# Kernel tuning notes

Hardware: AMD Instinct MI355X
Metric: run time of the kernel (lower is better)

Reference implementation:

```python
import jax, jax.numpy as jnp
import numpy as np

N, E, T = 10000, 50000, 80000   # nodes, edges, triplets
D, H, C, CF = 16, 128, 64, 64   # n_orb, hidden_dim, conv_dim, coeffs_dim


def l2norm(v):
    # matches torch F.normalize(dim=-1): x / max(||x||_2, 1e-12)
    return v / jnp.maximum(jnp.linalg.norm(v, axis=-1, keepdims=True), 1e-12)


def setup_inputs() -> dict:
    key = jax.random.key(0)
    ks = jax.random.split(key, 16)

    def w(k, i, o):
        return jax.random.normal(k, (i, o), jnp.float32) / np.sqrt(i).astype(np.float32)

    return {
        "x": jax.random.normal(ks[0], (N, H), jnp.float32),
        "cji": jax.random.normal(ks[1], (E, D, CF), jnp.float32),
        "robs": jax.random.normal(ks[2], (E, D), jnp.float32),
        "shbs": jax.random.normal(ks[3], (T, D), jnp.float32),
        "idx_i": jax.random.randint(ks[4], (E,), 0, N),
        "idx_j": jax.random.randint(ks[5], (E,), 0, N),
        "tri_idx_k": jax.random.randint(ks[6], (T,), 0, N),
        "edge_idx_kj": jax.random.randint(ks[7], (T,), 0, E),
        "edge_idx_ji": jax.random.randint(ks[8], (T,), 0, E),
        "W_nb": w(ks[9], H, 2 * C), "b_nb": jnp.zeros((2 * C,), jnp.float32),
        "W_c1": w(ks[10], CF, C),
        "W_c2": w(ks[11], C, 2 * C),
        "W_t3": w(ks[12], C, C), "b_t3": jnp.zeros((C,), jnp.float32),
        "W_n1": w(ks[13], 2 * C, C), "b_n1": jnp.zeros((C,), jnp.float32),
        "W_n2": w(ks[14], C, C), "b_n2": jnp.zeros((C,), jnp.float32),
        "W_na": w(ks[15], C, H),
    }


def reference(x, cji, robs, shbs, idx_i, idx_j, tri_idx_k, edge_idx_kj,
              edge_idx_ji, W_nb, b_nb, W_c1, W_c2, W_t3, b_t3, W_n1, b_n1,
              W_n2, b_n2, W_na):
    silu = jax.nn.silu
    # node_before_lin + chunk
    h = x @ W_nb + b_nb                       # [N, 2C]
    xq, xk = jnp.split(h, 2, axis=-1)         # each [N, C]
    # coeffs_before_lin: act -> Dense -> act -> Dense (no biases)
    c = silu(silu(cji) @ W_c1) @ W_c2         # [E, D, 2C]
    cji2, ckj = jnp.split(c, 2, axis=-1)      # each [E, D, C]
    # triplet gathers
    ckj_g = l2norm(ckj[edge_idx_kj])          # [T, D, C]
    tbo = l2norm(jnp.einsum('td,tdh->th', shbs * robs[edge_idx_kj], ckj_g))  # [T, C]
    tbw = tbo * jax.nn.sigmoid(xk[tri_idx_k])  # [T, C]
    # scatter triplets -> edges (dim_size = robs.size(0) = E)
    agg = jax.ops.segment_sum(tbw, edge_idx_ji, num_segments=E)  # [E, C]
    tbw2 = silu(agg) @ W_t3 + b_t3            # three_lin, [E, C]
    cji3 = l2norm(cji2 * (1.0 + tbw2[:, None, :]))  # cji + cji*w, normalized
    lcao = l2norm(jnp.einsum('ed,edh->eh', robs, cji3))  # [E, C]
    # node message: node_lin on concatenated endpoint features
    m = jnp.concatenate([xq[idx_i], xq[idx_j]], axis=-1)  # [E, 2C]
    m = silu(silu(m) @ W_n1 + b_n1) @ W_n2 + b_n2          # [E, C]
    out = x + jax.ops.segment_sum(lcao * m, idx_i, num_segments=N) @ W_na
    return out
```

## Files before the change

### kernel.cpp

```cpp
#include <hip/hip_runtime.h>
#include <hip/hip_bf16.h>

#define NN 10000
#define EE 50000
#define TT 80000
#define DD 16
#define HH 128
#define CC 64

typedef __hip_bfloat16 bf16;
typedef __attribute__((ext_vector_type(8))) short bf16x8;
typedef __attribute__((ext_vector_type(4))) float f32x4;

__device__ __forceinline__ float silu_f(float x) {
  return x * __builtin_amdgcn_rcpf(1.f + __expf(-x));
}
__device__ __forceinline__ float sigm_f(float x) {
  return __builtin_amdgcn_rcpf(1.f + __expf(-x));
}

__device__ __forceinline__ short f2bs(float x) {
  __hip_bfloat16 h = __float2bfloat16(x);
  short s;
  __builtin_memcpy(&s, &h, 2);
  return s;
}

__device__ __forceinline__ float rnorm_f(float ss) {
  return __builtin_amdgcn_rcpf(fmaxf(__builtin_amdgcn_sqrtf(ss), 1e-12f));
}

__device__ __forceinline__ void bf2x(unsigned u, float& lo, float& hi) {
  lo = __uint_as_float(u << 16);
  hi = __uint_as_float(u & 0xffff0000u);
}

#define ZERO_U4 960000
__global__ __launch_bounds__(256) void k_zero(uint4* __restrict__ p) {
  const int stride = gridDim.x * 256;
  for (int i = blockIdx.x * 256 + threadIdx.x; i < ZERO_U4; i += stride)
    p[i] = (uint4){0u, 0u, 0u, 0u};
}

__global__ __launch_bounds__(128) void k_node(
    const float* __restrict__ x, const float* __restrict__ W_nb,
    const float* __restrict__ b_nb, float* __restrict__ sxq,
    float* __restrict__ sigxk) {
  __shared__ __align__(16) float xs[8][HH];
  const int t = threadIdx.x;
  const int base = blockIdx.x * 8;
#pragma unroll
  for (int i = 0; i < 8; ++i) xs[i][t] = x[(size_t)(base + i) * HH + t];
  __syncthreads();
  float acc[8];
  const float bb = b_nb[t];
#pragma unroll
  for (int i = 0; i < 8; ++i) acc[i] = bb;
  for (int k = 0; k < HH; k += 4) {
    const float w0 = W_nb[(k + 0) * HH + t];
    const float w1 = W_nb[(k + 1) * HH + t];
    const float w2 = W_nb[(k + 2) * HH + t];
    const float w3 = W_nb[(k + 3) * HH + t];
#pragma unroll
    for (int i = 0; i < 8; ++i) {
      const float4 xv = *(const float4*)(&xs[i][k]);
      acc[i] = fmaf(xv.x, w0, acc[i]);
      acc[i] = fmaf(xv.y, w1, acc[i]);
      acc[i] = fmaf(xv.z, w2, acc[i]);
      acc[i] = fmaf(xv.w, w3, acc[i]);
    }
  }
  if (t < CC) {
#pragma unroll
    for (int i = 0; i < 8; ++i)
      sxq[(size_t)(base + i) * CC + t] = silu_f(acc[i]);
  } else {
#pragma unroll
    for (int i = 0; i < 8; ++i)
      sigxk[(size_t)(base + i) * CC + (t - CC)] = sigm_f(acc[i]);
  }
}

#define K2_BLOCKS 2048
#define K2_TILES 50000
__global__ __launch_bounds__(256, 2) void k_coeffs(
    const float* __restrict__ cji, const float* __restrict__ W_c1,
    const float* __restrict__ W_c2, bf16* __restrict__ cji2,
    bf16* __restrict__ ckjn) {
  __shared__ __align__(16) short xbuf[4][16 * 72];
  const int tid = threadIdx.x;
  const int w = tid >> 6, l = tid & 63;
  const int lr = l & 15, lg = l >> 4;
  short* mybuf = xbuf[w];

  bf16x8 b1[2][4];
  bf16x8 b2[2][8];
#pragma unroll
  for (int kt = 0; kt < 2; ++kt) {
#pragma unroll
    for (int nt = 0; nt < 4; ++nt) {
      bf16x8 t;
#pragma unroll
      for (int b = 0; b < 8; ++b)
        t[b] = f2bs(W_c1[(kt * 32 + lg * 8 + b) * 64 + nt * 16 + lr]);
      b1[kt][nt] = t;
    }
#pragma unroll
    for (int nt = 0; nt < 8; ++nt) {
      bf16x8 t;
#pragma unroll
      for (int b = 0; b < 8; ++b)
        t[b] = f2bs(W_c2[(kt * 32 + lg * 8 + b) * 128 + nt * 16 + lr]);
      b2[kt][nt] = t;
    }
  }

  const int nwave = K2_BLOCKS * 4;
  int tile = blockIdx.x * 4 + w;
  if (tile >= K2_TILES) return;

  float4 r0, r1, r2, r3;
  {
    const float* Ab = cji + (size_t)tile * 1024 + lr * 64 + lg * 8;
    r0 = *(const float4*)(Ab);
    r1 = *(const float4*)(Ab + 4);
    r2 = *(const float4*)(Ab + 32);
    r3 = *(const float4*)(Ab + 36);
  }

  for (; tile < K2_TILES; tile += nwave) {
    bf16x8 a0, a1;
    a0[0] = f2bs(silu_f(r0.x)); a0[1] = f2bs(silu_f(r0.y));
    a0[2] = f2bs(silu_f(r0.z)); a0[3] = f2bs(silu_f(r0.w));
    a0[4] = f2bs(silu_f(r1.x)); a0[5] = f2bs(silu_f(r1.y));
    a0[6] = f2bs(silu_f(r1.z)); a0[7] = f2bs(silu_f(r1.w));
    a1[0] = f2bs(silu_f(r2.x)); a1[1] = f2bs(silu_f(r2.y));
    a1[2] = f2bs(silu_f(r2.z)); a1[3] = f2bs(silu_f(r2.w));
    a1[4] = f2bs(silu_f(r3.x)); a1[5] = f2bs(silu_f(r3.y));
    a1[6] = f2bs(silu_f(r3.z)); a1[7] = f2bs(silu_f(r3.w));

    const int next = tile + nwave;
    if (next < K2_TILES) {
      const float* Ab = cji + (size_t)next * 1024 + lr * 64 + lg * 8;
      r0 = *(const float4*)(Ab);
      r1 = *(const float4*)(Ab + 4);
      r2 = *(const float4*)(Ab + 32);
      r3 = *(const float4*)(Ab + 36);
    }

    f32x4 acc1[4];
#pragma unroll
    for (int nt = 0; nt < 4; ++nt) acc1[nt] = (f32x4){0.f, 0.f, 0.f, 0.f};
#pragma unroll
    for (int nt = 0; nt < 4; ++nt) {
      acc1[nt] = __builtin_amdgcn_mfma_f32_16x16x32_bf16(a0, b1[0][nt], acc1[nt], 0, 0, 0);
      acc1[nt] = __builtin_amdgcn_mfma_f32_16x16x32_bf16(a1, b1[1][nt], acc1[nt], 0, 0, 0);
    }

#pragma unroll
    for (int nt = 0; nt < 4; ++nt)
#pragma unroll
      for (int j = 0; j < 4; ++j)
        mybuf[(lg * 4 + j) * 72 + nt * 16 + lr] = f2bs(silu_f(acc1[nt][j]));

    const bf16x8 a20 = *(const bf16x8*)(mybuf + lr * 72 + lg * 8);
    const bf16x8 a21 = *(const bf16x8*)(mybuf + lr * 72 + 32 + lg * 8);

    f32x4 acc2[8];
#pragma unroll
    for (int nt = 0; nt < 8; ++nt) acc2[nt] = (f32x4){0.f, 0.f, 0.f, 0.f};
#pragma unroll
    for (int nt = 0; nt < 8; ++nt) {
      acc2[nt] = __builtin_amdgcn_mfma_f32_16x16x32_bf16(a20, b2[0][nt], acc2[nt], 0, 0, 0);
      acc2[nt] = __builtin_amdgcn_mfma_f32_16x16x32_bf16(a21, b2[1][nt], acc2[nt], 0, 0, 0);
    }

    float rn[4];
#pragma unroll
    for (int j = 0; j < 4; ++j) {
      float ss = acc2[4][j] * acc2[4][j];
      ss = fmaf(acc2[5][j], acc2[5][j], ss);
      ss = fmaf(acc2[6][j], acc2[6][j], ss);
      ss = fmaf(acc2[7][j], acc2[7][j], ss);
#pragma unroll
      for (int m = 1; m < 16; m <<= 1) ss += __shfl_xor(ss, m, 64);
      rn[j] = rnorm_f(ss);
    }

    union { short h[16]; uint4 u[2]; } p;
#pragma unroll
    for (int nt = 0; nt < 4; ++nt)
#pragma unroll
      for (int j = 0; j < 4; ++j) p.h[nt * 4 + j] = f2bs(acc2[nt][j]);
    {
      uint4* d0 = (uint4*)(cji2 + (size_t)tile * 1024 + l * 16);
      d0[0] = p.u[0];
      d0[1] = p.u[1];
    }
#pragma unroll
    for (int nt = 0; nt < 4; ++nt)
#pragma unroll
      for (int j = 0; j < 4; ++j) p.h[nt * 4 + j] = f2bs(acc2[4 + nt][j] * rn[j]);
    {
      uint4* d1 = (uint4*)(ckjn + (size_t)tile * 1024 + l * 16);
      d1[0] = p.u[0];
      d1[1] = p.u[1];
    }
  }
}

#define K3_WAVES 20000
__global__ __launch_bounds__(256) void k_triplet(
    const bf16* __restrict__ ckjn, const float* __restrict__ shbs,
    const float* __restrict__ robs, const float* __restrict__ sigxk,
    const int* __restrict__ tri_idx_k, const int* __restrict__ edge_idx_kj,
    const int* __restrict__ edge_idx_ji, float* __restrict__ agg) {
  const int wid = (blockIdx.x * 256 + threadIdx.x) >> 6;
  const int l = threadIdx.x & 63;
  if (wid >= K3_WAVES) return;
  const int lq = l >> 4;
  const int t0 = wid * 4;

  int kj[4], kn[4], ji[4];
#pragma unroll
  for (int i = 0; i < 4; ++i) {
    kj[i] = edge_idx_kj[t0 + i];
    kn[i] = tri_idx_k[t0 + i];
    ji[i] = edge_idx_ji[t0 + i];
  }
  float4 sh[4], rb[4];
  uint4 u0[4], u1[4];
  float sx[4];
#pragma unroll
  for (int i = 0; i < 4; ++i) {
    sh[i] = *(const float4*)(shbs + (size_t)(t0 + i) * DD + lq * 4);
    rb[i] = *(const float4*)(robs + (size_t)kj[i] * DD + lq * 4);
    const uint4* b = (const uint4*)(ckjn + (size_t)kj[i] * 1024 + l * 16);
    u0[i] = b[0];
    u1[i] = b[1];
    sx[i] = sigxk[(size_t)kn[i] * CC + l];
  }

  float acc[4][4];
#pragma unroll
  for (int i = 0; i < 4; ++i) {
    const float w0 = sh[i].x * rb[i].x, w1 = sh[i].y * rb[i].y,
                w2 = sh[i].z * rb[i].z, w3 = sh[i].w * rb[i].w;
    float x0, x1, x2, x3;
    bf2x(u0[i].x, x0, x1); bf2x(u0[i].y, x2, x3);
    acc[i][0] = fmaf(w3, x3, fmaf(w2, x2, fmaf(w1, x1, w0 * x0)));
    bf2x(u0[i].z, x0, x1); bf2x(u0[i].w, x2, x3);
    acc[i][1] = fmaf(w3, x3, fmaf(w2, x2, fmaf(w1, x1, w0 * x0)));
    bf2x(u1[i].x, x0, x1); bf2x(u1[i].y, x2, x3);
    acc[i][2] = fmaf(w3, x3, fmaf(w2, x2, fmaf(w1, x1, w0 * x0)));
    bf2x(u1[i].z, x0, x1); bf2x(u1[i].w, x2, x3);
    acc[i][3] = fmaf(w3, x3, fmaf(w2, x2, fmaf(w1, x1, w0 * x0)));
  }
#pragma unroll
  for (int m = 16; m < 64; m <<= 1)
#pragma unroll
    for (int i = 0; i < 4; ++i)
#pragma unroll
      for (int q = 0; q < 4; ++q) acc[i][q] += __shfl_xor(acc[i][q], m, 64);

  float sel[4], ss[4];
#pragma unroll
  for (int i = 0; i < 4; ++i) {
    sel[i] = (lq == 0) ? acc[i][0] : (lq == 1) ? acc[i][1]
             : (lq == 2) ? acc[i][2] : acc[i][3];
    ss[i] = sel[i] * sel[i];
  }
#pragma unroll
  for (int m = 1; m < 64; m <<= 1)
#pragma unroll
    for (int i = 0; i < 4; ++i) ss[i] += __shfl_xor(ss[i], m, 64);
#pragma unroll
  for (int i = 0; i < 4; ++i) {
    const float tbw = sel[i] * rnorm_f(ss[i]) * sx[i];
    atomicAdd(&agg[(size_t)ji[i] * CC + l], tbw);
  }
}

#define K4A_TILES 3125
#define K4A_BLOCKS 256
__global__ __launch_bounds__(256, 2) void k_edge_a(
    const float* __restrict__ agg, const float* __restrict__ sxq,
    const int* __restrict__ idx_i, const int* __restrict__ idx_j,
    const float* __restrict__ W_t3, const float* __restrict__ b_t3,
    const float* __restrict__ W_n1, const float* __restrict__ b_n1,
    const float* __restrict__ W_n2, const float* __restrict__ b_n2,
    float* __restrict__ onew_buf, float* __restrict__ m_buf) {
  __shared__ __align__(16) float fbuf[4][16 * 68];
  __shared__ __align__(16) short sbuf[4][16 * 72];
  const int tid = threadIdx.x;
  const int w = tid >> 6, l = tid & 63;
  const int lr = l & 15, lg = l >> 4;
  float* fb = fbuf[w];
  short* sb = sbuf[w];

  bf16x8 bt3[2][4], bn1[4][4], bn2[2][4];
#pragma unroll
  for (int kt = 0; kt < 2; ++kt)
#pragma unroll
    for (int nt = 0; nt < 4; ++nt) {
      bf16x8 t;
#pragma unroll
      for (int b = 0; b < 8; ++b)
        t[b] = f2bs(W_t3[(kt * 32 + lg * 8 + b) * 64 + nt * 16 + lr]);
      bt3[kt][nt] = t;
    }
#pragma unroll
  for (int kt = 0; kt < 4; ++kt)
#pragma unroll
    for (int nt = 0; nt < 4; ++nt) {
      bf16x8 t;
#pragma unroll
      for (int b = 0; b < 8; ++b)
        t[b] = f2bs(W_n1[(kt * 32 + lg * 8 + b) * 64 + nt * 16 + lr]);
      bn1[kt][nt] = t;
    }
#pragma unroll
  for (int kt = 0; kt < 2; ++kt)
#pragma unroll
    for (int nt = 0; nt < 4; ++nt) {
      bf16x8 t;
#pragma unroll
      for (int b = 0; b < 8; ++b)
        t[b] = f2bs(W_n2[(kt * 32 + lg * 8 + b) * 64 + nt * 16 + lr]);
      bn2[kt][nt] = t;
    }
  float bt3c[4], bn1c[4], bn2c[4];
#pragma unroll
  for (int nt = 0; nt < 4; ++nt) {
    bt3c[nt] = b_t3[nt * 16 + lr];
    bn1c[nt] = b_n1[nt * 16 + lr];
    bn2c[nt] = b_n2[nt * 16 + lr];
  }

  for (int tile = blockIdx.x * 4 + w; tile < K4A_TILES; tile += K4A_BLOCKS * 4) {
    const int e = tile * 16 + lr;
    const int vi = idx_i[e], vj = idx_j[e];

    bf16x8 aagg[2];
#pragma unroll
    for (int kt = 0; kt < 2; ++kt) {
      const float4 u = *(const float4*)(agg + (size_t)e * 64 + kt * 32 + lg * 8);
      const float4 v = *(const float4*)(agg + (size_t)e * 64 + kt * 32 + lg * 8 + 4);
      bf16x8 t;
      t[0] = f2bs(silu_f(u.x)); t[1] = f2bs(silu_f(u.y));
      t[2] = f2bs(silu_f(u.z)); t[3] = f2bs(silu_f(u.w));
      t[4] = f2bs(silu_f(v.x)); t[5] = f2bs(silu_f(v.y));
      t[6] = f2bs(silu_f(v.z)); t[7] = f2bs(silu_f(v.w));
      aagg[kt] = t;
    }
    f32x4 acc[4];
#pragma unroll
    for (int nt = 0; nt < 4; ++nt) acc[nt] = (f32x4){0.f, 0.f, 0.f, 0.f};
#pragma unroll
    for (int nt = 0; nt < 4; ++nt) {
      acc[nt] = __builtin_amdgcn_mfma_f32_16x16x32_bf16(aagg[0], bt3[0][nt], acc[nt], 0, 0, 0);
      acc[nt] = __builtin_amdgcn_mfma_f32_16x16x32_bf16(aagg[1], bt3[1][nt], acc[nt], 0, 0, 0);
    }
#pragma unroll
    for (int nt = 0; nt < 4; ++nt)
#pragma unroll
      for (int j = 0; j < 4; ++j)
        fb[(lg * 4 + j) * 68 + nt * 16 + lr] = 1.f + bt3c[nt] + acc[nt][j];
    {
      const int row = l >> 2, cs = (l & 3) * 16;
      float* dst = onew_buf + (size_t)(tile * 16 + row) * 64 + cs;
#pragma unroll
      for (int q = 0; q < 4; ++q)
        *(float4*)(dst + q * 4) = *(const float4*)(fb + row * 68 + cs + q * 4);
    }

    bf16x8 am[4];
#pragma unroll
    for (int kt = 0; kt < 4; ++kt) {
      const float* src = (kt < 2) ? (sxq + (size_t)vi * 64 + kt * 32)
                                  : (sxq + (size_t)vj * 64 + (kt - 2) * 32);
      const float4 u = *(const float4*)(src + lg * 8);
      const float4 v = *(const float4*)(src + lg * 8 + 4);
      bf16x8 t;
      t[0] = f2bs(u.x); t[1] = f2bs(u.y); t[2] = f2bs(u.z); t[3] = f2bs(u.w);
      t[4] = f2bs(v.x); t[5] = f2bs(v.y); t[6] = f2bs(v.z); t[7] = f2bs(v.w);
      am[kt] = t;
    }
    f32x4 acc1[4];
#pragma unroll
    for (int nt = 0; nt < 4; ++nt) acc1[nt] = (f32x4){0.f, 0.f, 0.f, 0.f};
#pragma unroll
    for (int nt = 0; nt < 4; ++nt)
#pragma unroll
      for (int kt = 0; kt < 4; ++kt)
        acc1[nt] = __builtin_amdgcn_mfma_f32_16x16x32_bf16(am[kt], bn1[kt][nt], acc1[nt], 0, 0, 0);

#pragma unroll
    for (int nt = 0; nt < 4; ++nt)
#pragma unroll
      for (int j = 0; j < 4; ++j)
        sb[(lg * 4 + j) * 72 + nt * 16 + lr] = f2bs(silu_f(acc1[nt][j] + bn1c[nt]));
    const bf16x8 a20 = *(const bf16x8*)(sb + lr * 72 + lg * 8);
    const bf16x8 a21 = *(const bf16x8*)(sb + lr * 72 + 32 + lg * 8);

    f32x4 acc2[4];
#pragma unroll
    for (int nt = 0; nt < 4; ++nt) acc2[nt] = (f32x4){0.f, 0.f, 0.f, 0.f};
#pragma unroll
    for (int nt = 0; nt < 4; ++nt) {
      acc2[nt] = __builtin_amdgcn_mfma_f32_16x16x32_bf16(a20, bn2[0][nt], acc2[nt], 0, 0, 0);
      acc2[nt] = __builtin_amdgcn_mfma_f32_16x16x32_bf16(a21, bn2[1][nt], acc2[nt], 0, 0, 0);
    }
#pragma unroll
    for (int nt = 0; nt < 4; ++nt)
#pragma unroll
      for (int j = 0; j < 4; ++j)
        fb[(lg * 4 + j) * 68 + nt * 16 + lr] = acc2[nt][j] + bn2c[nt];
    {
      const int row = l >> 2, cs = (l & 3) * 16;
      float* dst = m_buf + (size_t)(tile * 16 + row) * 64 + cs;
#pragma unroll
      for (int q = 0; q < 4; ++q)
        *(float4*)(dst + q * 4) = *(const float4*)(fb + row * 68 + cs + q * 4);
    }
  }
}

#define K4B_WAVES 25000
__global__ __launch_bounds__(256) void k_edge_b(
    const bf16* __restrict__ cji2, const float* __restrict__ robs,
    const float* __restrict__ onew_buf, const float* __restrict__ m_buf,
    const int* __restrict__ idx_i, float* __restrict__ lacc) {
  const int wid = (blockIdx.x * 256 + threadIdx.x) >> 6;
  const int l = threadIdx.x & 63;
  if (wid >= K4B_WAVES) return;
  const int lq = l >> 4, lr = l & 15;
  const int e0 = wid * 2;

  uint4 u0[2], u1[2];
  float4 rb[2];
  float ow[2][4], mm[2];
  int vi[2];
#pragma unroll
  for (int i = 0; i < 2; ++i) {
    const uint4* base = (const uint4*)(cji2 + (size_t)(e0 + i) * 1024 + l * 16);
    u0[i] = base[0];
    u1[i] = base[1];
    const float* ob = onew_buf + (size_t)(e0 + i) * 64 + lr;
    ow[i][0] = ob[0]; ow[i][1] = ob[16]; ow[i][2] = ob[32]; ow[i][3] = ob[48];
    rb[i] = *(const float4*)(robs + (size_t)(e0 + i) * DD + lq * 4);
    mm[i] = m_buf[(size_t)(e0 + i) * 64 + l];
    vi[i] = idx_i[e0 + i];
  }

  float v[2][16];
#pragma unroll
  for (int i = 0; i < 2; ++i) {
    bf2x(u0[i].x, v[i][0], v[i][1]);   bf2x(u0[i].y, v[i][2], v[i][3]);
    bf2x(u0[i].z, v[i][4], v[i][5]);   bf2x(u0[i].w, v[i][6], v[i][7]);
    bf2x(u1[i].x, v[i][8], v[i][9]);   bf2x(u1[i].y, v[i][10], v[i][11]);
    bf2x(u1[i].z, v[i][12], v[i][13]); bf2x(u1[i].w, v[i][14], v[i][15]);
#pragma unroll
    for (int j = 0; j < 4; ++j) {
      v[i][j] *= ow[i][0];
      v[i][4 + j] *= ow[i][1];
      v[i][8 + j] *= ow[i][2];
      v[i][12 + j] *= ow[i][3];
    }
  }
  float sq[2][4];
#pragma unroll
  for (int i = 0; i < 2; ++i)
#pragma unroll
    for (int j = 0; j < 4; ++j)
      sq[i][j] = fmaf(v[i][j], v[i][j],
                 fmaf(v[i][4 + j], v[i][4 + j],
                 fmaf(v[i][8 + j], v[i][8 + j], v[i][12 + j] * v[i][12 + j])));
#pragma unroll
  for (int m = 1; m < 16; m <<= 1)
#pragma unroll
    for (int i = 0; i < 2; ++i)
#pragma unroll
      for (int j = 0; j < 4; ++j) sq[i][j] += __shfl_xor(sq[i][j], m, 64);

  float lcq[2][4];
#pragma unroll
  for (int i = 0; i < 2; ++i) {
    const float t0 = rb[i].x * rnorm_f(sq[i][0]),
                t1 = rb[i].y * rnorm_f(sq[i][1]),
                t2 = rb[i].z * rnorm_f(sq[i][2]),
                t3 = rb[i].w * rnorm_f(sq[i][3]);
#pragma unroll
    for (int q = 0; q < 4; ++q)
      lcq[i][q] = fmaf(t0, v[i][q * 4 + 0],
                  fmaf(t1, v[i][q * 4 + 1],
                  fmaf(t2, v[i][q * 4 + 2], t3 * v[i][q * 4 + 3])));
  }
#pragma unroll
  for (int m = 16; m < 64; m <<= 1)
#pragma unroll
    for (int i = 0; i < 2; ++i)
#pragma unroll
      for (int q = 0; q < 4; ++q) lcq[i][q] += __shfl_xor(lcq[i][q], m, 64);

  float sel[2], ss[2];
#pragma unroll
  for (int i = 0; i < 2; ++i) {
    sel[i] = (lq == 0) ? lcq[i][0] : (lq == 1) ? lcq[i][1]
             : (lq == 2) ? lcq[i][2] : lcq[i][3];
    ss[i] = sel[i] * sel[i];
  }
#pragma unroll
  for (int m = 1; m < 64; m <<= 1)
#pragma unroll
    for (int i = 0; i < 2; ++i) ss[i] += __shfl_xor(ss[i], m, 64);
#pragma unroll
  for (int i = 0; i < 2; ++i) {
    const float lcao = sel[i] * rnorm_f(ss[i]);
    atomicAdd(&lacc[(size_t)vi[i] * CC + l], lcao * mm[i]);
  }
}

__global__ __launch_bounds__(128) void k_out(
    const float* __restrict__ x, const float* __restrict__ lacc,
    const float* __restrict__ W_na, float* __restrict__ out) {
  __shared__ __align__(16) float ls[8][CC];
  const int t = threadIdx.x;
  const int base = blockIdx.x * 8;
  for (int idx = t; idx < 8 * CC; idx += 128)
    ls[idx >> 6][idx & 63] = lacc[(size_t)(base + (idx >> 6)) * CC + (idx & 63)];
  __syncthreads();
  float acc[8];
#pragma unroll
  for (int i = 0; i < 8; ++i) acc[i] = x[(size_t)(base + i) * HH + t];
  for (int k = 0; k < CC; k += 4) {
    const float w0 = W_na[(k + 0) * HH + t];
    const float w1 = W_na[(k + 1) * HH + t];
    const float w2 = W_na[(k + 2) * HH + t];
    const float w3 = W_na[(k + 3) * HH + t];
#pragma unroll
    for (int i = 0; i < 8; ++i) {
      const float4 lv = *(const float4*)(&ls[i][k]);
      acc[i] = fmaf(lv.x, w0, acc[i]);
      acc[i] = fmaf(lv.y, w1, acc[i]);
      acc[i] = fmaf(lv.z, w2, acc[i]);
      acc[i] = fmaf(lv.w, w3, acc[i]);
    }
  }
#pragma unroll
  for (int i = 0; i < 8; ++i) out[(size_t)(base + i) * HH + t] = acc[i];
}

extern "C" void kernel_launch(void* const* d_in, const int* in_sizes, int n_in,
                              void* d_out, int out_size, void* d_ws,
                              size_t ws_size, hipStream_t stream) {
  const float* x = (const float*)d_in[0];
  const float* cji = (const float*)d_in[1];
  const float* robs = (const float*)d_in[2];
  const float* shbs = (const float*)d_in[3];
  const int* idx_i = (const int*)d_in[4];
  const int* idx_j = (const int*)d_in[5];
  const int* tri_idx_k = (const int*)d_in[6];
  const int* edge_idx_kj = (const int*)d_in[7];
  const int* edge_idx_ji = (const int*)d_in[8];
  const float* W_nb = (const float*)d_in[9];
  const float* b_nb = (const float*)d_in[10];
  const float* W_c1 = (const float*)d_in[11];
  const float* W_c2 = (const float*)d_in[12];
  const float* W_t3 = (const float*)d_in[13];
  const float* b_t3 = (const float*)d_in[14];
  const float* W_n1 = (const float*)d_in[15];
  const float* b_n1 = (const float*)d_in[16];
  const float* W_n2 = (const float*)d_in[17];
  const float* b_n2 = (const float*)d_in[18];
  const float* W_na = (const float*)d_in[19];
  float* out = (float*)d_out;

  char* ws = (char*)d_ws;
  const size_t NC4 = (size_t)NN * CC * 4;
  const size_t EDC2 = (size_t)EE * DD * CC * 2;
  const size_t EC4 = (size_t)EE * CC * 4;
  float* sxq = (float*)(ws);
  float* sigxk = (float*)(ws + NC4);
  bf16* cji2 = (bf16*)(ws + 2 * NC4);
  bf16* ckjn = (bf16*)(ws + 2 * NC4 + EDC2);
  float* agg = (float*)(ws + 2 * NC4 + 2 * EDC2);
  float* lacc = (float*)(ws + 2 * NC4 + 2 * EDC2 + EC4);
  float* onew_buf = (float*)(ws + 2 * NC4 + EDC2);
  float* m_buf = (float*)(ws + 2 * NC4 + EDC2 + EC4);

  k_zero<<<1024, 256, 0, stream>>>((uint4*)agg);

  k_node<<<NN / 8, 128, 0, stream>>>(x, W_nb, b_nb, sxq, sigxk);
  k_coeffs<<<K2_BLOCKS, 256, 0, stream>>>(cji, W_c1, W_c2, cji2, ckjn);
  k_triplet<<<(K3_WAVES + 3) / 4, 256, 0, stream>>>(ckjn, shbs, robs, sigxk,
                                                    tri_idx_k, edge_idx_kj,
                                                    edge_idx_ji, agg);
  k_edge_a<<<K4A_BLOCKS, 256, 0, stream>>>(
      agg, sxq, idx_i, idx_j, W_t3, b_t3, W_n1, b_n1, W_n2, b_n2, onew_buf,
      m_buf);
  k_edge_b<<<(K4B_WAVES + 3) / 4, 256, 0, stream>>>(cji2, robs, onew_buf,
                                                    m_buf, idx_i, lacc);
  k_out<<<NN / 8, 128, 0, stream>>>(x, lacc, W_na, out);
}
```

Baseline: 200.4 us.

## Chain coeff MLP MFMAs in registers via transposed 16x16x16 layout, drop LDS

Recasts the two-layer coefficient MLP in k_coeffs so the first GEMM computes the transposed product (W1^T times activations) with 16x16x16 bf16 MFMAs. Its accumulator layout then serves directly as the A operand of the second GEMM, which removes the per-tile LDS round trip used to re-layout the hidden activations. Input loads are reshaped to match the new K-split. The cost is twice as many, smaller MFMA instructions and changed weight-register packing, with the same overall work.

```diff
diff --git a/kernel.cpp b/kernel.cpp
--- a/kernel.cpp
+++ b/kernel.cpp
@@ -10,6 +10,7 @@
 
 typedef __hip_bfloat16 bf16;
 typedef __attribute__((ext_vector_type(8))) short bf16x8;
+typedef __attribute__((ext_vector_type(4))) short bf16x4;
 typedef __attribute__((ext_vector_type(4))) float f32x4;
 
 __device__ __forceinline__ float silu_f(float x) {
@@ -87,93 +88,87 @@
     const float* __restrict__ cji, const float* __restrict__ W_c1,
     const float* __restrict__ W_c2, bf16* __restrict__ cji2,
     bf16* __restrict__ ckjn) {
-  __shared__ __align__(16) short xbuf[4][16 * 72];
   const int tid = threadIdx.x;
   const int w = tid >> 6, l = tid & 63;
   const int lr = l & 15, lg = l >> 4;
-  short* mybuf = xbuf[w];
-
-  bf16x8 b1[2][4];
-  bf16x8 b2[2][8];
-#pragma unroll
-  for (int kt = 0; kt < 2; ++kt) {
-#pragma unroll
-    for (int nt = 0; nt < 4; ++nt) {
-      bf16x8 t;
-#pragma unroll
-      for (int b = 0; b < 8; ++b)
-        t[b] = f2bs(W_c1[(kt * 32 + lg * 8 + b) * 64 + nt * 16 + lr]);
-      b1[kt][nt] = t;
-    }
-#pragma unroll
-    for (int nt = 0; nt < 8; ++nt) {
-      bf16x8 t;
-#pragma unroll
-      for (int b = 0; b < 8; ++b)
-        t[b] = f2bs(W_c2[(kt * 32 + lg * 8 + b) * 128 + nt * 16 + lr]);
-      b2[kt][nt] = t;
-    }
-  }
+
+  bf16x4 bw1[4][4];
+  bf16x4 bw2[4][8];
+#pragma unroll
+  for (int rt = 0; rt < 4; ++rt)
+#pragma unroll
+    for (int kt = 0; kt < 4; ++kt) {
+      bf16x4 t;
+#pragma unroll
+      for (int b = 0; b < 4; ++b)
+        t[b] = f2bs(W_c1[(kt * 16 + lg * 4 + b) * 64 + rt * 16 + lr]);
+      bw1[rt][kt] = t;
+    }
+#pragma unroll
+  for (int kt = 0; kt < 4; ++kt)
+#pragma unroll
+    for (int ct = 0; ct < 8; ++ct) {
+      bf16x4 t;
+#pragma unroll
+      for (int b = 0; b < 4; ++b)
+        t[b] = f2bs(W_c2[(kt * 16 + lg * 4 + b) * 128 + ct * 16 + lr]);
+      bw2[kt][ct] = t;
+    }
 
   const int nwave = K2_BLOCKS * 4;
   int tile = blockIdx.x * 4 + w;
   if (tile >= K2_TILES) return;
 
-  float4 r0, r1, r2, r3;
-  {
-    const float* Ab = cji + (size_t)tile * 1024 + lr * 64 + lg * 8;
-    r0 = *(const float4*)(Ab);
-    r1 = *(const float4*)(Ab + 4);
-    r2 = *(const float4*)(Ab + 32);
-    r3 = *(const float4*)(Ab + 36);
-  }
+  float4 r[4];
+#pragma unroll
+  for (int kt = 0; kt < 4; ++kt)
+    r[kt] = *(const float4*)(cji + (size_t)tile * 1024 + lr * 64 + kt * 16 + lg * 4);
 
   for (; tile < K2_TILES; tile += nwave) {
-    bf16x8 a0, a1;
-    a0[0] = f2bs(silu_f(r0.x)); a0[1] = f2bs(silu_f(r0.y));
-    a0[2] = f2bs(silu_f(r0.z)); a0[3] = f2bs(silu_f(r0.w));
-    a0[4] = f2bs(silu_f(r1.x)); a0[5] = f2bs(silu_f(r1.y));
-    a0[6] = f2bs(silu_f(r1.z)); a0[7] = f2bs(silu_f(r1.w));
-    a1[0] = f2bs(silu_f(r2.x)); a1[1] = f2bs(silu_f(r2.y));
-    a1[2] = f2bs(silu_f(r2.z)); a1[3] = f2bs(silu_f(r2.w));
-    a1[4] = f2bs(silu_f(r3.x)); a1[5] = f2bs(silu_f(r3.y));
-    a1[6] = f2bs(silu_f(r3.z)); a1[7] = f2bs(silu_f(r3.w));
+    bf16x4 sB[4];
+#pragma unroll
+    for (int kt = 0; kt < 4; ++kt) {
+      bf16x4 t;
+      t[0] = f2bs(silu_f(r[kt].x));
+      t[1] = f2bs(silu_f(r[kt].y));
+      t[2] = f2bs(silu_f(r[kt].z));
+      t[3] = f2bs(silu_f(r[kt].w));
+      sB[kt] = t;
+    }
 
     const int next = tile + nwave;
     if (next < K2_TILES) {
-      const float* Ab = cji + (size_t)next * 1024 + lr * 64 + lg * 8;
-      r0 = *(const float4*)(Ab);
-      r1 = *(const float4*)(Ab + 4);
-      r2 = *(const float4*)(Ab + 32);
-      r3 = *(const float4*)(Ab + 36);
+#pragma unroll
+      for (int kt = 0; kt < 4; ++kt)
+        r[kt] = *(const float4*)(cji + (size_t)next * 1024 + lr * 64 + kt * 16 + lg * 4);
     }
 
     f32x4 acc1[4];
 #pragma unroll
-    for (int nt = 0; nt < 4; ++nt) acc1[nt] = (f32x4){0.f, 0.f, 0.f, 0.f};
-#pragma unroll
-    for (int nt = 0; nt < 4; ++nt) {
-      acc1[nt] = __builtin_amdgcn_mfma_f32_16x16x32_bf16(a0, b1[0][nt], acc1[nt], 0, 0, 0);
-      acc1[nt] = __builtin_amdgcn_mfma_f32_16x16x32_bf16(a1, b1[1][nt], acc1[nt], 0, 0, 0);
-    }
-
-#pragma unroll
-    for (int nt = 0; nt < 4; ++nt)
-#pragma unroll
-      for (int j = 0; j < 4; ++j)
-        mybuf[(lg * 4 + j) * 72 + nt * 16 + lr] = f2bs(silu_f(acc1[nt][j]));
-
-    const bf16x8 a20 = *(const bf16x8*)(mybuf + lr * 72 + lg * 8);
-    const bf16x8 a21 = *(const bf16x8*)(mybuf + lr * 72 + 32 + lg * 8);
+    for (int rt = 0; rt < 4; ++rt) acc1[rt] = (f32x4){0.f, 0.f, 0.f, 0.f};
+#pragma unroll
+    for (int rt = 0; rt < 4; ++rt)
+#pragma unroll
+      for (int kt = 0; kt < 4; ++kt)
+        acc1[rt] = __builtin_amdgcn_mfma_f32_16x16x16bf16_1k(bw1[rt][kt], sB[kt], acc1[rt], 0, 0, 0);
+
+    bf16x4 tf[4];
+#pragma unroll
+    for (int kt = 0; kt < 4; ++kt) {
+      bf16x4 t;
+#pragma unroll
+      for (int b = 0; b < 4; ++b) t[b] = f2bs(silu_f(acc1[kt][b]));
+      tf[kt] = t;
+    }
 
     f32x4 acc2[8];
 #pragma unroll
-    for (int nt = 0; nt < 8; ++nt) acc2[nt] = (f32x4){0.f, 0.f, 0.f, 0.f};
-#pragma unroll
-    for (int nt = 0; nt < 8; ++nt) {
-      acc2[nt] = __builtin_amdgcn_mfma_f32_16x16x32_bf16(a20, b2[0][nt], acc2[nt], 0, 0, 0);
-      acc2[nt] = __builtin_amdgcn_mfma_f32_16x16x32_bf16(a21, b2[1][nt], acc2[nt], 0, 0, 0);
-    }
+    for (int ct = 0; ct < 8; ++ct) acc2[ct] = (f32x4){0.f, 0.f, 0.f, 0.f};
+#pragma unroll
+    for (int ct = 0; ct < 8; ++ct)
+#pragma unroll
+      for (int kt = 0; kt < 4; ++kt)
+        acc2[ct] = __builtin_amdgcn_mfma_f32_16x16x16bf16_1k(tf[kt], bw2[kt][ct], acc2[ct], 0, 0, 0);
 
     float rn[4];
 #pragma unroll
@@ -189,18 +184,18 @@
 
     union { short h[16]; uint4 u[2]; } p;
 #pragma unroll
-    for (int nt = 0; nt < 4; ++nt)
-#pragma unroll
-      for (int j = 0; j < 4; ++j) p.h[nt * 4 + j] = f2bs(acc2[nt][j]);
+    for (int ct = 0; ct < 4; ++ct)
+#pragma unroll
+      for (int j = 0; j < 4; ++j) p.h[ct * 4 + j] = f2bs(acc2[ct][j]);
     {
       uint4* d0 = (uint4*)(cji2 + (size_t)tile * 1024 + l * 16);
       d0[0] = p.u[0];
       d0[1] = p.u[1];
     }
 #pragma unroll
-    for (int nt = 0; nt < 4; ++nt)
-#pragma unroll
-      for (int j = 0; j < 4; ++j) p.h[nt * 4 + j] = f2bs(acc2[4 + nt][j] * rn[j]);
+    for (int ct = 0; ct < 4; ++ct)
+#pragma unroll
+      for (int j = 0; j < 4; ++j) p.h[ct * 4 + j] = f2bs(acc2[4 + ct][j] * rn[j]);
     {
       uint4* d1 = (uint4*)(ckjn + (size_t)tile * 1024 + l * 16);
       d1[0] = p.u[0];
```

New measurement: 201.5 us. About the same (+0.6%).
